# Kernel optimization log

Hardware: AMD Instinct MI355X
Metric: run time of the kernel (lower is better)

Reference implementation:

```python
import jax, jax.numpy as jnp
import numpy as np

B, F, BLOCK = 8192, 3072, 3


def _det3(a):
    # analytic determinant of (..., 3, 3)
    return (a[..., 0, 0] * (a[..., 1, 1] * a[..., 2, 2] - a[..., 1, 2] * a[..., 2, 1])
            - a[..., 0, 1] * (a[..., 1, 0] * a[..., 2, 2] - a[..., 1, 2] * a[..., 2, 0])
            + a[..., 0, 2] * (a[..., 1, 0] * a[..., 2, 1] - a[..., 1, 1] * a[..., 2, 0]))


def setup_inputs() -> dict:
    key = jax.random.key(0)
    k1, k2 = jax.random.split(key)
    x = jax.random.normal(k1, (B, F), dtype=jnp.float32)
    # w must be strictly inside the unit sphere per block: normalize to radius 0.5
    g = jax.random.normal(k2, (B, F), dtype=jnp.float32).reshape(B, F // BLOCK, BLOCK)
    g = 0.5 * g / jnp.linalg.norm(g, axis=-1, keepdims=True)
    return {"x": x, "w": g.reshape(B, F), "blocks": BLOCK}


def _moebius(x, w, block):
    batch, nfeat = x.shape
    nb = nfeat // block
    xb = x.reshape(batch, nb, block)   # (B, nb, d)
    wb = w.reshape(batch, nb, block)
    x_norm = jnp.sqrt(jnp.sum(xb * xb, axis=-1, keepdims=True))        # (B, nb, 1)
    xn = xb / x_norm                                                   # normalized x
    xpw = xn + wb
    wns = jnp.sum(wb * wb, axis=-1, keepdims=True)                     # |w|^2
    xwns = jnp.sum(xpw * xpw, axis=-1, keepdims=True)                  # |xn+w|^2
    yn = (1.0 - wns) / xwns * xpw + wb                                 # y_normalized
    y = x_norm * yn

    # block Jacobian dy/dx, shape (B, nb, d, d)
    eye = jnp.eye(block, dtype=x.dtype)
    xn4 = x_norm[..., None]            # (B, nb, 1, 1)
    dxn_dx = (eye - xb[..., :, None] * xb[..., None, :] / (xn4 * xn4)) / xn4
    g = jnp.einsum('bnij,bnj->bni', dxn_dx, xpw)
    J = (2.0 / xwns[..., None]) * (xpw[..., :, None] * g[..., None, :])
    J = xn4 * (1.0 - wns[..., None]) / xwns[..., None] * (dxn_dx - J)
    J = J + yn[..., :, None] * xn[..., None, :]

    log_det_J = jnp.sum(jnp.log(jnp.abs(_det3(J))), axis=1)            # (B,)
    return y.reshape(batch, nfeat), log_det_J


def reference(x, w, blocks):
    return _moebius(x, w, blocks)
```

## Files before the change

kernel.cpp:

```cpp
#include <hip/hip_runtime.h>
#include <math.h>

#define BATCH 8192
#define FEAT  3072
#define NBLK  1024
#define TPB   256
#define BPT   4

__global__ __launch_bounds__(TPB, 4)
void moebius_kernel(const float* __restrict__ x,
                    const float* __restrict__ w,
                    float* __restrict__ out) {
    __shared__ float sx[FEAT];
    __shared__ float sw[FEAT];
    __shared__ float swred[TPB / 64];

    const int row = blockIdx.x;
    const int tid = threadIdx.x;

    const float4* __restrict__ x4 = (const float4*)(x + (size_t)row * FEAT);
    const float4* __restrict__ w4 = (const float4*)(w + (size_t)row * FEAT);
    float4* sx4 = (float4*)sx;
    float4* sw4 = (float4*)sw;

    #pragma unroll
    for (int i = 0; i < 3; ++i) {
        sx4[tid + i * TPB] = x4[tid + i * TPB];
        sw4[tid + i * TPB] = w4[tid + i * TPB];
    }
    __syncthreads();

    float lsum = 0.0f;

    #pragma unroll
    for (int j = 0; j < BPT; ++j) {
        const int k = tid + j * TPB;
        const int base = 3 * k;

        const float x0 = sx[base], x1 = sx[base + 1], x2 = sx[base + 2];
        const float w0 = sw[base], w1 = sw[base + 1], w2 = sw[base + 2];

        const float r2    = x0 * x0 + x1 * x1 + x2 * x2;
        const float r     = sqrtf(r2);
        const float inv_r = 1.0f / r;
        const float xn0 = x0 * inv_r, xn1 = x1 * inv_r, xn2 = x2 * inv_r;

        const float p0 = xn0 + w0, p1 = xn1 + w1, p2 = xn2 + w2;
        const float wns  = w0 * w0 + w1 * w1 + w2 * w2;
        const float xwns = p0 * p0 + p1 * p1 + p2 * p2;
        const float inv_xwns = 1.0f / xwns;
        const float c = (1.0f - wns) * inv_xwns;

        const float yn0 = c * p0 + w0;
        const float yn1 = c * p1 + w1;
        const float yn2 = c * p2 + w2;

        sx[base]     = r * yn0;
        sx[base + 1] = r * yn1;
        sx[base + 2] = r * yn2;

        const float s  = xn0 * p0 + xn1 * p1 + xn2 * p2;
        const float t2 = 2.0f * inv_xwns;
        const float q0 = p0 - s * xn0;
        const float q1 = p1 - s * xn1;
        const float q2 = p2 - s * xn2;

        const float J00 = c * (1.0f - xn0 * xn0 - t2 * p0 * q0) + yn0 * xn0;
        const float J01 = c * (       - xn0 * xn1 - t2 * p0 * q1) + yn0 * xn1;
        const float J02 = c * (       - xn0 * xn2 - t2 * p0 * q2) + yn0 * xn2;
        const float J10 = c * (       - xn1 * xn0 - t2 * p1 * q0) + yn1 * xn0;
        const float J11 = c * (1.0f - xn1 * xn1 - t2 * p1 * q1) + yn1 * xn1;
        const float J12 = c * (       - xn1 * xn2 - t2 * p1 * q2) + yn1 * xn2;
        const float J20 = c * (       - xn2 * xn0 - t2 * p2 * q0) + yn2 * xn0;
        const float J21 = c * (       - xn2 * xn1 - t2 * p2 * q1) + yn2 * xn1;
        const float J22 = c * (1.0f - xn2 * xn2 - t2 * p2 * q2) + yn2 * xn2;

        const float det = J00 * (J11 * J22 - J12 * J21)
                        - J01 * (J10 * J22 - J12 * J20)
                        + J02 * (J10 * J21 - J11 * J20);

        lsum += logf(fabsf(det));
    }

    __syncthreads();

    float4* y4 = (float4*)(out + (size_t)row * FEAT);
    #pragma unroll
    for (int i = 0; i < 3; ++i) {
        y4[tid + i * TPB] = sx4[tid + i * TPB];
    }

    #pragma unroll
    for (int off = 32; off > 0; off >>= 1) {
        lsum += __shfl_down(lsum, off, 64);
    }
    const int lane = tid & 63;
    const int wave = tid >> 6;
    if (lane == 0) swred[wave] = lsum;
    __syncthreads();
    if (tid == 0) {
        float tot = swred[0] + swred[1] + swred[2] + swred[3];
        out[(size_t)BATCH * FEAT + row] = tot;
    }
}

extern "C" void kernel_launch(void* const* d_in, const int* in_sizes, int n_in,
                              void* d_out, int out_size, void* d_ws, size_t ws_size,
                              hipStream_t stream) {
    const float* x = (const float*)d_in[0];
    const float* w = (const float*)d_in[1];
    float* out = (float*)d_out;

    moebius_kernel<<<BATCH, TPB, 0, stream>>>(x, w, out);
}
```

Baseline: 243.3 us.

## Replace 3x3 Jacobian determinant with closed-form log of Möbius scale factor

Computes log|det J| analytically as 2·ln(c), where c = (1-|w|^2)/|xn+w|^2, using a log2 intrinsic scaled by 2·ln2. This removes the per-block 3x3 Jacobian build and its determinant. The shared-memory staging of x and w is also dropped in favour of direct strided global loads and stores, and the occupancy hint is raised from 4 to 8. It also swaps in hardware rsq/rcp/log2 intrinsics, which are slightly less precise than the original sqrt, division and logf, and the strided scalar accesses may coalesce less well than the float4 copies.

```diff
diff --git a/kernel.cpp b/kernel.cpp
--- a/kernel.cpp
+++ b/kernel.cpp
@@ -7,87 +7,46 @@
 #define TPB   256
 #define BPT   4
 
-__global__ __launch_bounds__(TPB, 4)
+
+__global__ __launch_bounds__(TPB, 8)
 void moebius_kernel(const float* __restrict__ x,
                     const float* __restrict__ w,
                     float* __restrict__ out) {
-    __shared__ float sx[FEAT];
-    __shared__ float sw[FEAT];
     __shared__ float swred[TPB / 64];
 
     const int row = blockIdx.x;
     const int tid = threadIdx.x;
-
-    const float4* __restrict__ x4 = (const float4*)(x + (size_t)row * FEAT);
-    const float4* __restrict__ w4 = (const float4*)(w + (size_t)row * FEAT);
-    float4* sx4 = (float4*)sx;
-    float4* sw4 = (float4*)sw;
-
-    #pragma unroll
-    for (int i = 0; i < 3; ++i) {
-        sx4[tid + i * TPB] = x4[tid + i * TPB];
-        sw4[tid + i * TPB] = w4[tid + i * TPB];
-    }
-    __syncthreads();
+    const size_t rb = (size_t)row * FEAT;
 
     float lsum = 0.0f;
 
     #pragma unroll
     for (int j = 0; j < BPT; ++j) {
         const int k = tid + j * TPB;
-        const int base = 3 * k;
+        const float* __restrict__ xp = x + rb + 3 * k;
+        const float* __restrict__ wp = w + rb + 3 * k;
 
-        const float x0 = sx[base], x1 = sx[base + 1], x2 = sx[base + 2];
-        const float w0 = sw[base], w1 = sw[base + 1], w2 = sw[base + 2];
+        const float x0 = xp[0], x1 = xp[1], x2 = xp[2];
+        const float w0 = wp[0], w1 = wp[1], w2 = wp[2];
 
-        const float r2    = x0 * x0 + x1 * x1 + x2 * x2;
-        const float r     = sqrtf(r2);
-        const float inv_r = 1.0f / r;
-        const float xn0 = x0 * inv_r, xn1 = x1 * inv_r, xn2 = x2 * inv_r;
+        const float r2   = x0 * x0 + x1 * x1 + x2 * x2;
+        const float invr = __builtin_amdgcn_rsqf(r2);
+        const float r    = r2 * invr;
 
-        const float p0 = xn0 + w0, p1 = xn1 + w1, p2 = xn2 + w2;
+        const float p0 = x0 * invr + w0;
+        const float p1 = x1 * invr + w1;
+        const float p2 = x2 * invr + w2;
+
         const float wns  = w0 * w0 + w1 * w1 + w2 * w2;
         const float xwns = p0 * p0 + p1 * p1 + p2 * p2;
-        const float inv_xwns = 1.0f / xwns;
-        const float c = (1.0f - wns) * inv_xwns;
+        const float c    = (1.0f - wns) * __builtin_amdgcn_rcpf(xwns);
 
-        const float yn0 = c * p0 + w0;
-        const float yn1 = c * p1 + w1;
-        const float yn2 = c * p2 + w2;
+        float* __restrict__ yp = out + rb + 3 * k;
+        yp[0] = r * (c * p0 + w0);
+        yp[1] = r * (c * p1 + w1);
+        yp[2] = r * (c * p2 + w2);
 
-        sx[base]     = r * yn0;
-        sx[base + 1] = r * yn1;
-        sx[base + 2] = r * yn2;
-
-        const float s  = xn0 * p0 + xn1 * p1 + xn2 * p2;
-        const float t2 = 2.0f * inv_xwns;
-        const float q0 = p0 - s * xn0;
-        const float q1 = p1 - s * xn1;
-        const float q2 = p2 - s * xn2;
-
-        const float J00 = c * (1.0f - xn0 * xn0 - t2 * p0 * q0) + yn0 * xn0;
-        const float J01 = c * (       - xn0 * xn1 - t2 * p0 * q1) + yn0 * xn1;
-        const float J02 = c * (       - xn0 * xn2 - t2 * p0 * q2) + yn0 * xn2;
-        const float J10 = c * (       - xn1 * xn0 - t2 * p1 * q0) + yn1 * xn0;
-        const float J11 = c * (1.0f - xn1 * xn1 - t2 * p1 * q1) + yn1 * xn1;
-        const float J12 = c * (       - xn1 * xn2 - t2 * p1 * q2) + yn1 * xn2;
-        const float J20 = c * (       - xn2 * xn0 - t2 * p2 * q0) + yn2 * xn0;
-        const float J21 = c * (       - xn2 * xn1 - t2 * p2 * q1) + yn2 * xn1;
-        const float J22 = c * (1.0f - xn2 * xn2 - t2 * p2 * q2) + yn2 * xn2;
-
-        const float det = J00 * (J11 * J22 - J12 * J21)
-                        - J01 * (J10 * J22 - J12 * J20)
-                        + J02 * (J10 * J21 - J11 * J20);
-
-        lsum += logf(fabsf(det));
-    }
-
-    __syncthreads();
-
-    float4* y4 = (float4*)(out + (size_t)row * FEAT);
-    #pragma unroll
-    for (int i = 0; i < 3; ++i) {
-        y4[tid + i * TPB] = sx4[tid + i * TPB];
+        lsum += __builtin_amdgcn_logf(c);
     }
 
     #pragma unroll
@@ -99,7 +58,7 @@
     if (lane == 0) swred[wave] = lsum;
     __syncthreads();
     if (tid == 0) {
-        float tot = swred[0] + swred[1] + swred[2] + swred[3];
+        const float tot = (swred[0] + swred[1] + swred[2] + swred[3]) * 1.3862943611f;
         out[(size_t)BATCH * FEAT + row] = tot;
     }
 }
```

After: 241.7 us. No clear change (-0.7%).
